# Kernel tuning notes

Hardware: AMD Instinct MI355X
Metric: run time of the kernel (lower is better)

## Reference

```python
import jax, jax.numpy as jnp
import numpy as np
import math

VOCAB, EMBED, RES = 50257, 512, 2048
B, T = 64, 512
LN_EPS = 1e-5


def setup_inputs() -> dict:
    key = jax.random.key(0)
    k_x, k_e, k_r, k_w = jax.random.split(key, 4)
    x = jax.random.randint(k_x, (B, T), 0, VOCAB)
    embed_weight = jax.random.normal(k_e, (VOCAB, EMBED), dtype=jnp.float32)
    R = jax.random.normal(k_r, (RES, RES), dtype=jnp.float32) / math.sqrt(RES) / 0.9
    Win = jax.random.normal(k_w, (EMBED, RES), dtype=jnp.float32) / math.sqrt(EMBED) / 0.9
    gamma = jnp.ones((RES,), dtype=jnp.float32)
    beta = jnp.zeros((RES,), dtype=jnp.float32)
    return {"x": x, "embed_weight": embed_weight, "R": R, "Win": Win,
            "gamma": gamma, "beta": beta}


def reference(x, embed_weight, R, Win, gamma, beta):
    emb = embed_weight[x]                              # [B, T, E]
    inp = jnp.einsum('bte,er->btr', emb, Win)          # [B, T, RES]

    def step(state, u_t):                              # state: [B, RES]
        new_state = jnp.tanh(state @ R + u_t)
        return new_state, None

    state0 = jnp.zeros((x.shape[0], R.shape[0]), dtype=emb.dtype)
    state, _ = jax.lax.scan(step, state0, jnp.swapaxes(inp, 0, 1))  # scan over T

    # LayerNorm over last dim (eps=1e-5, affine)
    mu = jnp.mean(state, axis=-1, keepdims=True)
    var = jnp.mean((state - mu) ** 2, axis=-1, keepdims=True)
    normed = (state - mu) / jnp.sqrt(var + LN_EPS)
    return normed * gamma + beta
```

## Files before the change

kernel.cpp:

```cpp
#include <hip/hip_runtime.h>

#define BB 64
#define TT 512
#define EE 512
#define RR 2048
#define CPW 32
#define RPG 16
#define NWGS 256
#define FPAD 16

typedef _Float16 f16;
typedef f16 f16x8 __attribute__((ext_vector_type(8)));
typedef float f32x4 __attribute__((ext_vector_type(4)));

__device__ __forceinline__ void gload16(const void* g, void* l) {
  __builtin_amdgcn_global_load_lds(
      (const __attribute__((address_space(1))) void*)g,
      (__attribute__((address_space(3))) void*)l, 16, 0, 0);
}

__device__ __forceinline__ float fast_tanh(float v) {
  float e = __expf(2.0f * v);
  return 1.0f - 2.0f / (e + 1.0f);
}

__device__ __forceinline__ void storeS(f16* p, float v) {
  union { f16 h; unsigned short s; } u;
  u.h = (f16)v;
  __hip_atomic_store((unsigned short*)p, u.s, __ATOMIC_RELAXED, __HIP_MEMORY_SCOPE_AGENT);
}

__device__ __forceinline__ unsigned flag_ld(const unsigned* p) {
  return __hip_atomic_load(p, __ATOMIC_RELAXED, __HIP_MEMORY_SCOPE_AGENT);
}
__device__ __forceinline__ void flag_st(unsigned* p, unsigned v) {
  __hip_atomic_store(p, v, __ATOMIC_RELAXED, __HIP_MEMORY_SCOPE_AGENT);
}

__device__ __forceinline__ void issue8(f16x8* dst, unsigned voff, const f16* sbase) {
#pragma unroll
  for (int i = 0; i < 8; ++i)
    asm volatile("global_load_dwordx4 %0, %1, %2 offset:%c3 sc0"
                 : "=v"(dst[i]) : "v"(voff), "s"(sbase), "i"(64 * i) : "memory");
}

__device__ __forceinline__ unsigned bypass_ld(unsigned voff, const unsigned* base) {
  unsigned v;
  asm volatile("global_load_dword %0, %1, %2 sc0 sc1"
               : "=v"(v) : "v"(voff), "s"(base) : "memory");
  return v;
}

template <int N>
__device__ __forceinline__ void wait_vm() {
  asm volatile("s_waitcnt vmcnt(%c0)" :: "i"(N) : "memory");
  __builtin_amdgcn_sched_barrier(0);
}


__global__ void prep_emb(const int* __restrict__ x, const float* __restrict__ ew,
                         f16* __restrict__ emb) {
  const int row = blockIdx.x;
  const int tok = x[row];
  const float4* src = (const float4*)(ew + (size_t)tok * EE);
  f16* dst = emb + (size_t)row * EE;
  const int i = threadIdx.x;
  float4 v = src[i];
  union { f16 h[4]; unsigned long long u; } p;
  p.h[0] = (f16)v.x; p.h[1] = (f16)v.y; p.h[2] = (f16)v.z; p.h[3] = (f16)v.w;
  ((unsigned long long*)dst)[i] = p.u;
}

__global__ void prep_winT(const float* __restrict__ Win, f16* __restrict__ WinT) {
  const int i = blockIdx.x * blockDim.x + threadIdx.x;
  if (i < EE * RR) {
    const int k = i / RR, n = i % RR;
    WinT[(size_t)n * EE + k] = (f16)Win[i];
  }
}


__launch_bounds__(256, 1)
__global__ void proj_gemm(const f16* __restrict__ A, const f16* __restrict__ Bt,
                          float* __restrict__ U) {
  __shared__ f16 As[128 * 32];
  __shared__ f16 Bs[128 * 32];
  const int tid = threadIdx.x;
  const int wv = tid >> 6, l = tid & 63;
  const int m0 = blockIdx.x * 128, n0 = blockIdx.y * 128;
  const int wm = wv >> 1, wn = wv & 1;
  const int srow = tid >> 2, sc = tid & 3;
  const int r = l & 15, kb = l >> 4;
  f32x4 acc[4][4] = {};

  for (int k0 = 0; k0 < EE; k0 += 32) {
    __syncthreads();
#pragma unroll
    for (int q = 0; q < 2; ++q) {
      const int row = q * 64 + srow;
      const int cc = sc ^ (row & 3);
      gload16(A + (size_t)(m0 + row) * EE + k0 + cc * 8,
              (char*)As + q * 4096 + wv * 1024);
      gload16(Bt + (size_t)(n0 + row) * EE + k0 + cc * 8,
              (char*)Bs + q * 4096 + wv * 1024);
    }
    __syncthreads();
    f16x8 af[4], bf[4];
#pragma unroll
    for (int mi = 0; mi < 4; ++mi) {
      const int row = wm * 64 + mi * 16 + r;
      af[mi] = *(const f16x8*)&As[row * 32 + ((kb ^ (row & 3)) * 8)];
    }
#pragma unroll
    for (int ni = 0; ni < 4; ++ni) {
      const int row = wn * 64 + ni * 16 + r;
      bf[ni] = *(const f16x8*)&Bs[row * 32 + ((kb ^ (row & 3)) * 8)];
    }
#pragma unroll
    for (int mi = 0; mi < 4; ++mi)
#pragma unroll
      for (int ni = 0; ni < 4; ++ni)
        acc[mi][ni] = __builtin_amdgcn_mfma_f32_16x16x32_f16(af[mi], bf[ni], acc[mi][ni], 0, 0, 0);
  }
  const int rb = kb * 4;
#pragma unroll
  for (int mi = 0; mi < 4; ++mi)
#pragma unroll
    for (int ni = 0; ni < 4; ++ni)
#pragma unroll
      for (int j = 0; j < 4; ++j) {
        const int m = m0 + wm * 64 + mi * 16 + rb + j;
        const int n = n0 + wn * 64 + ni * 16 + r;
        const int b = m >> 9, t = m & 511;
        __builtin_nontemporal_store(acc[mi][ni][j], &U[(size_t)(t * BB + b) * RR + n]);
      }
}


__launch_bounds__(576, 1)
__global__ void scan_kernel(const float* __restrict__ R, const float* __restrict__ U,
                            f16* __restrict__ S, unsigned* __restrict__ flg,
                            unsigned* __restrict__ fflag) {
  __shared__ __align__(16) char ldsbuf[CPW * RR * 2 + 16 * 1040];
  f16* Rt = (f16*)ldsbuf;
  const char* RtB = (const char*)ldsbuf;

  const int wg = blockIdx.x;
  const int xcd = wg & 7;
  const int grp = xcd >> 1;
  const int cw = ((wg >> 3) << 1) | (wg & 1);
  const bool leader = (wg >> 3) == 0;
  const int nbase = cw * CPW;
  const int rbase = grp * RPG;
  const int tid = threadIdx.x;
  const int wv = tid >> 6, l = tid & 63;
  unsigned* gflags = flg + grp * 64 * FPAD;
  unsigned* myflag = gflags + cw * FPAD;
  unsigned* myff = fflag + xcd * FPAD;

  const int mm = tid >> 5, cc = tid & 31;
  if (tid < 512)
    storeS(&S[(size_t)(BB * RR) + (size_t)(rbase + mm) * RR + nbase + cc],
           fast_tanh(U[(size_t)(rbase + mm) * RR + nbase + cc]));
  __syncthreads();
  if (tid == 0) flag_st(myflag, 1u);

  if (tid < 512) {
    const int c = tid & 31, kst = tid >> 5;
    for (int k = kst; k < RR; k += 16) {
      const float v = R[(size_t)k * RR + nbase + c];
      const int idx = ((k >> 5) << 10) + ((c >> 4) << 9) +
                      (((c & 15) << 2) + ((k >> 3) & 3)) * 8 + (k & 7);
      Rt[idx] = (f16)v;
    }
  }
  __syncthreads();

  if (wv < 8) {
    const int r = l & 15, kb = l >> 4;
    const int kblk = (wv + cw) & 7;
    const unsigned voffA = (unsigned)((((rbase + r) * RR) + (kblk << 8) + kb * 8) * 2);
    const int bb0 = (r * 4 + kb) * 16;
    const unsigned poff = (unsigned)(((grp * 64 + kblk * 8 + (l & 7)) * FPAD) * 4);
    const unsigned foff = (unsigned)((xcd * FPAD) * 4);
    const int ntr = cc >> 4;
    const int lred = (cc & 15) | ((mm >> 2) << 4);
    const int jred = mm & 3;

    f16x8 abuf[8];

    for (int tau = 2; tau <= TT; ++tau) {
      const f16* sprev = S + (size_t)((tau - 1) & 1) * (BB * RR);
      f16* snext = S + (size_t)(tau & 1) * (BB * RR);
      const unsigned need = (unsigned)(tau - 1);

      unsigned ffv = bypass_ld(foff, fflag);
      unsigned pv0 = bypass_ld(poff, flg);
      unsigned pv1 = bypass_ld(poff, flg);
      for (;;) {
        wait_vm<1>();
        if (__all(pv0 >= need)) break;
        pv0 = bypass_ld(poff, flg);
        wait_vm<1>();
        if (__all(pv1 >= need)) break;
        pv1 = bypass_ld(poff, flg);
        __builtin_amdgcn_s_sleep(0);
      }
      wait_vm<0>();
      while (ffv < (unsigned)tau) {
        __builtin_amdgcn_s_sleep(1);
        ffv = flag_ld(myff);
      }

      issue8(abuf, voffA, sprev);
      const float uval = __builtin_nontemporal_load(
          &U[(size_t)(tau - 1) * (BB * RR) + (size_t)(rbase + mm) * RR + nbase + cc]);

      f32x4 acc0 = {0.f, 0.f, 0.f, 0.f}, acc1 = {0.f, 0.f, 0.f, 0.f};
#define KSTEP(ks)                                                              \
  {                                                                            \
    const int kc = (kblk << 3) + (ks);                                         \
    f16x8 b0 = *(const f16x8*)(RtB + kc * 2048 + bb0);                         \
    f16x8 b1 = *(const f16x8*)(RtB + kc * 2048 + 1024 + bb0);                  \
    acc0 = __builtin_amdgcn_mfma_f32_16x16x32_f16(abuf[ks], b0, acc0, 0, 0, 0);\
    acc1 = __builtin_amdgcn_mfma_f32_16x16x32_f16(abuf[ks], b1, acc1, 0, 0, 0);\
  }
      wait_vm<5>();
      KSTEP(0) KSTEP(1) KSTEP(2) KSTEP(3)
      wait_vm<1>();
      KSTEP(4) KSTEP(5) KSTEP(6) KSTEP(7)
#undef KSTEP

      {
        char* red = ldsbuf + CPW * RR * 2;
        *(f32x4*)(red + (wv * 2 + 0) * 1040 + l * 16) = acc0;
        *(f32x4*)(red + (wv * 2 + 1) * 1040 + l * 16) = acc1;
      }
      __syncthreads();
      {
        const char* red = ldsbuf + CPW * RR * 2;
        float s = 0.f;
#pragma unroll
        for (int w = 0; w < 8; ++w)
          s += *(const float*)(red + (w * 2 + ntr) * 1040 + lred * 16 + jred * 4);
        storeS(&snext[(size_t)(rbase + mm) * RR + nbase + cc], fast_tanh(s + uval));
      }
      __syncthreads();
      if (tid == 0) flag_st(myflag, (unsigned)tau);
    }
  } else {
    if (leader) {
      __builtin_amdgcn_fence(__ATOMIC_ACQUIRE, "agent");
      if (l == 0) flag_st(myff, 2u);
    }
    for (int tau = 2; tau <= TT; ++tau) {
      __syncthreads();
      if (leader && tau < TT) {
        __builtin_amdgcn_fence(__ATOMIC_ACQUIRE, "agent");
        if (l == 0) flag_st(myff, (unsigned)(tau + 1));
      }
      __syncthreads();
    }
  }
}


__launch_bounds__(256, 1)
__global__ void ln_kernel(const f16* __restrict__ Sfin, const float* __restrict__ gamma,
                          const float* __restrict__ beta, float* __restrict__ out) {
  const int b = blockIdx.x;
  const int tid = threadIdx.x;
  const f16* row = Sfin + (size_t)b * RR;
  float vals[8];
  float lsum = 0.f, lsq = 0.f;
#pragma unroll
  for (int i = 0; i < 8; ++i) {
    float v = (float)row[tid + i * 256];
    vals[i] = v; lsum += v; lsq += v * v;
  }
#pragma unroll
  for (int off = 32; off >= 1; off >>= 1) {
    lsum += __shfl_xor(lsum, off);
    lsq  += __shfl_xor(lsq, off);
  }
  __shared__ float ps[4], pq[4];
  __shared__ float mu_s, rstd_s;
  const int wv = tid >> 6, l = tid & 63;
  if (l == 0) { ps[wv] = lsum; pq[wv] = lsq; }
  __syncthreads();
  if (tid == 0) {
    float s = 0.f, q = 0.f;
    for (int i = 0; i < 4; ++i) { s += ps[i]; q += pq[i]; }
    const float mu = s / RR;
    const float var = q / RR - mu * mu;
    mu_s = mu; rstd_s = rsqrtf(var + 1e-5f);
  }
  __syncthreads();
  const float mu = mu_s, rstd = rstd_s;
#pragma unroll
  for (int i = 0; i < 8; ++i) {
    const int idx = tid + i * 256;
    out[(size_t)b * RR + idx] = (vals[i] - mu) * rstd * gamma[idx] + beta[idx];
  }
}


extern "C" void kernel_launch(void* const* d_in, const int* in_sizes, int n_in,
                              void* d_out, int out_size, void* d_ws, size_t ws_size,
                              hipStream_t stream) {
  const int*   x     = (const int*)d_in[0];
  const float* ew    = (const float*)d_in[1];
  const float* Rm    = (const float*)d_in[2];
  const float* Win   = (const float*)d_in[3];
  const float* gamma = (const float*)d_in[4];
  const float* beta  = (const float*)d_in[5];

  const size_t U_OFF   = 0;
  const size_t EMB_OFF = 268435456;
  const size_t WT_OFF  = EMB_OFF + 33554432;
  const size_t S_OFF   = WT_OFF + 2097152;
  const size_t BAR_OFF = S_OFF + 524288;
  const size_t FF_OFF  = BAR_OFF + 16384;
  const size_t NEED    = FF_OFF + 1024;
  if (ws_size < NEED) {
    hipMemsetAsync(d_out, 0, (size_t)out_size * 4, stream);
    return;
  }
  char* ws = (char*)d_ws;
  float*    Ubuf  = (float*)(ws + U_OFF);
  f16*      emb   = (f16*)(ws + EMB_OFF);
  f16*      WinT  = (f16*)(ws + WT_OFF);
  f16*      Sbuf  = (f16*)(ws + S_OFF);
  unsigned* flg   = (unsigned*)(ws + BAR_OFF);
  unsigned* fflag = (unsigned*)(ws + FF_OFF);

  hipMemsetAsync(flg, 0, 16384 + 1024, stream);
  prep_emb<<<BB * TT, 128, 0, stream>>>(x, ew, emb);
  prep_winT<<<(EE * RR) / 256, 256, 0, stream>>>(Win, WinT);
  proj_gemm<<<dim3((BB * TT) / 128, RR / 128), 256, 0, stream>>>(emb, WinT, Ubuf);
  scan_kernel<<<NWGS, 576, 0, stream>>>(Rm, Ubuf, Sbuf, flg, fflag);
  ln_kernel<<<BB, 256, 0, stream>>>(Sbuf, gamma, beta, (float*)d_out);
}
```

Before: 1.999 ms.

## Move cross-workgroup flag polling to a dedicated wave with LDS release signaling

The ninth wave now polls the global per-group flags and the XCD fence flag, then publishes a release counter in LDS. The eight compute waves spin on that LDS value instead of issuing global bypass loads, and __syncthreads is replaced by an LDS atomic-counter wave barrier. The next step's U value is also prefetched one iteration ahead. The aim is to take global-memory polling latency and full-block barriers off the recurrence critical path. In exchange it adds LDS spin traffic, bounded spin caps that could silently break ordering if they expire, and subtle memory-ordering risk.

Result: slower. 2.764 ms (+38.3%).

```diff
diff --git a/kernel.cpp b/kernel.cpp
--- a/kernel.cpp
+++ b/kernel.cpp
@@ -8,6 +8,7 @@
 #define RPG 16
 #define NWGS 256
 #define FPAD 16
+#define SPIN_CAP (1 << 18)
 
 typedef _Float16 f16;
 typedef f16 f16x8 __attribute__((ext_vector_type(8)));
@@ -24,9 +25,9 @@
   return 1.0f - 2.0f / (e + 1.0f);
 }
 
-__device__ __forceinline__ void storeS(f16* p, float v) {
+__device__ __forceinline__ void storeS(f16* p, f16 h) {
   union { f16 h; unsigned short s; } u;
-  u.h = (f16)v;
+  u.h = h;
   __hip_atomic_store((unsigned short*)p, u.s, __ATOMIC_RELAXED, __HIP_MEMORY_SCOPE_AGENT);
 }
 
@@ -44,16 +45,22 @@
                  : "=v"(dst[i]) : "v"(voff), "s"(sbase), "i"(64 * i) : "memory");
 }
 
-__device__ __forceinline__ unsigned bypass_ld(unsigned voff, const unsigned* base) {
-  unsigned v;
-  asm volatile("global_load_dword %0, %1, %2 sc0 sc1"
-               : "=v"(v) : "v"(voff), "s"(base) : "memory");
-  return v;
-}
-
 template <int N>
 __device__ __forceinline__ void wait_vm() {
   asm volatile("s_waitcnt vmcnt(%c0)" :: "i"(N) : "memory");
+  __builtin_amdgcn_sched_barrier(0);
+}
+
+__device__ __forceinline__ void wbar(unsigned* cnt, unsigned target, int lane) {
+  asm volatile("s_waitcnt lgkmcnt(0)" ::: "memory");
+  __builtin_amdgcn_sched_barrier(0);
+  if (lane == 0)
+    __hip_atomic_fetch_add(cnt, 1u, __ATOMIC_RELAXED, __HIP_MEMORY_SCOPE_WORKGROUP);
+  unsigned v;
+  int gd = 0;
+  do {
+    v = __hip_atomic_load(cnt, __ATOMIC_RELAXED, __HIP_MEMORY_SCOPE_WORKGROUP);
+  } while (v < target && ++gd < (1 << 22));
   __builtin_amdgcn_sched_barrier(0);
 }
 
@@ -142,6 +149,7 @@
                             f16* __restrict__ S, unsigned* __restrict__ flg,
                             unsigned* __restrict__ fflag) {
   __shared__ __align__(16) char ldsbuf[CPW * RR * 2 + 16 * 1040];
+  __shared__ unsigned wcnt, rel;
   f16* Rt = (f16*)ldsbuf;
   const char* RtB = (const char*)ldsbuf;
 
@@ -154,14 +162,17 @@
   const int rbase = grp * RPG;
   const int tid = threadIdx.x;
   const int wv = tid >> 6, l = tid & 63;
-  unsigned* gflags = flg + grp * 64 * FPAD;
+  unsigned* gflags = flg + (size_t)grp * 64 * FPAD;
   unsigned* myflag = gflags + cw * FPAD;
   unsigned* myff = fflag + xcd * FPAD;
 
+  if (tid == 0) { wcnt = 0u; rel = 1u; }
+
   const int mm = tid >> 5, cc = tid & 31;
-  if (tid < 512)
-    storeS(&S[(size_t)(BB * RR) + (size_t)(rbase + mm) * RR + nbase + cc],
-           fast_tanh(U[(size_t)(rbase + mm) * RR + nbase + cc]));
+  if (tid < 512) {
+    f16 h = (f16)fast_tanh(U[(size_t)(rbase + mm) * RR + nbase + cc]);
+    storeS(&S[(size_t)(BB * RR) + (size_t)(rbase + mm) * RR + nbase + cc], h);
+  }
   __syncthreads();
   if (tid == 0) flag_st(myflag, 1u);
 
@@ -181,40 +192,37 @@
     const int kblk = (wv + cw) & 7;
     const unsigned voffA = (unsigned)((((rbase + r) * RR) + (kblk << 8) + kb * 8) * 2);
     const int bb0 = (r * 4 + kb) * 16;
-    const unsigned poff = (unsigned)(((grp * 64 + kblk * 8 + (l & 7)) * FPAD) * 4);
-    const unsigned foff = (unsigned)((xcd * FPAD) * 4);
     const int ntr = cc >> 4;
     const int lred = (cc & 15) | ((mm >> 2) << 4);
     const int jred = mm & 3;
+    const unsigned ubase = (unsigned)(((rbase + mm) * RR + nbase + cc) * 4);
 
     f16x8 abuf[8];
+    unsigned btgt = 0;
+
+    float ucur;
+    asm volatile("global_load_dword %0, %1, %2 nt"
+                 : "=v"(ucur) : "v"(ubase + (unsigned)(1 * BB * RR * 4)), "s"(U) : "memory");
+    wait_vm<0>();
 
     for (int tau = 2; tau <= TT; ++tau) {
       const f16* sprev = S + (size_t)((tau - 1) & 1) * (BB * RR);
       f16* snext = S + (size_t)(tau & 1) * (BB * RR);
-      const unsigned need = (unsigned)(tau - 1);
-
-      unsigned ffv = bypass_ld(foff, fflag);
-      unsigned pv0 = bypass_ld(poff, flg);
-      unsigned pv1 = bypass_ld(poff, flg);
-      for (;;) {
-        wait_vm<1>();
-        if (__all(pv0 >= need)) break;
-        pv0 = bypass_ld(poff, flg);
-        wait_vm<1>();
-        if (__all(pv1 >= need)) break;
-        pv1 = bypass_ld(poff, flg);
-        __builtin_amdgcn_s_sleep(0);
-      }
-      wait_vm<0>();
-      while (ffv < (unsigned)tau) {
-        __builtin_amdgcn_s_sleep(1);
-        ffv = flag_ld(myff);
+
+      {
+        unsigned v; int gd = 0;
+        do {
+          v = __hip_atomic_load(&rel, __ATOMIC_RELAXED, __HIP_MEMORY_SCOPE_WORKGROUP);
+        } while (v < (unsigned)tau && ++gd < (1 << 22));
       }
 
       issue8(abuf, voffA, sprev);
-      const float uval = __builtin_nontemporal_load(
-          &U[(size_t)(tau - 1) * (BB * RR) + (size_t)(rbase + mm) * RR + nbase + cc]);
+      float unxt;
+      {
+        const int tn = (tau < TT) ? tau : TT - 1;
+        asm volatile("global_load_dword %0, %1, %2 nt"
+                     : "=v"(unxt) : "v"(ubase + (unsigned)(tn * BB * RR * 4)), "s"(U) : "memory");
+      }
 
       f32x4 acc0 = {0.f, 0.f, 0.f, 0.f}, acc1 = {0.f, 0.f, 0.f, 0.f};
 #define KSTEP(ks)                                                              \
@@ -236,30 +244,52 @@
         *(f32x4*)(red + (wv * 2 + 0) * 1040 + l * 16) = acc0;
         *(f32x4*)(red + (wv * 2 + 1) * 1040 + l * 16) = acc1;
       }
-      __syncthreads();
+      wbar(&wcnt, btgt += 8, l);
       {
         const char* red = ldsbuf + CPW * RR * 2;
         float s = 0.f;
 #pragma unroll
         for (int w = 0; w < 8; ++w)
           s += *(const float*)(red + (w * 2 + ntr) * 1040 + lred * 16 + jred * 4);
-        storeS(&snext[(size_t)(rbase + mm) * RR + nbase + cc], fast_tanh(s + uval));
-      }
-      __syncthreads();
+        storeS(&snext[(size_t)(rbase + mm) * RR + nbase + cc],
+               (f16)fast_tanh(s + ucur));
+      }
+      wait_vm<0>();
+      wbar(&wcnt, btgt += 8, l);
       if (tid == 0) flag_st(myflag, (unsigned)tau);
+      ucur = unxt;
     }
   } else {
+    const unsigned* pollp = &gflags[(size_t)l * FPAD];
     if (leader) {
       __builtin_amdgcn_fence(__ATOMIC_ACQUIRE, "agent");
       if (l == 0) flag_st(myff, 2u);
     }
     for (int tau = 2; tau <= TT; ++tau) {
-      __syncthreads();
-      if (leader && tau < TT) {
-        __builtin_amdgcn_fence(__ATOMIC_ACQUIRE, "agent");
-        if (l == 0) flag_st(myff, (unsigned)(tau + 1));
-      }
-      __syncthreads();
+      const unsigned need = (unsigned)(tau - 1);
+      {
+        unsigned fv = flag_ld(pollp);
+        int gd = 0;
+        while (!__all(fv >= need) && ++gd < SPIN_CAP) {
+          __builtin_amdgcn_s_sleep(1);
+          fv = flag_ld(pollp);
+        }
+      }
+      if (leader) {
+        if (tau > 2) {
+          __builtin_amdgcn_fence(__ATOMIC_ACQUIRE, "agent");
+          if (l == 0) flag_st(myff, (unsigned)tau);
+        }
+      } else {
+        unsigned ffv = flag_ld(myff);
+        int gd = 0;
+        while (ffv < (unsigned)tau && ++gd < SPIN_CAP) {
+          __builtin_amdgcn_s_sleep(1);
+          ffv = flag_ld(myff);
+        }
+      }
+      __hip_atomic_store(&rel, (unsigned)tau, __ATOMIC_RELAXED,
+                         __HIP_MEMORY_SCOPE_WORKGROUP);
     }
   }
 }
@@ -319,8 +349,8 @@
   const size_t EMB_OFF = 268435456;
   const size_t WT_OFF  = EMB_OFF + 33554432;
   const size_t S_OFF   = WT_OFF + 2097152;
-  const size_t BAR_OFF = S_OFF + 524288;
-  const size_t FF_OFF  = BAR_OFF + 16384;
+  const size_t FLG_OFF = S_OFF + 524288;
+  const size_t FF_OFF  = FLG_OFF + 16384;
   const size_t NEED    = FF_OFF + 1024;
   if (ws_size < NEED) {
     hipMemsetAsync(d_out, 0, (size_t)out_size * 4, stream);
@@ -331,7 +361,7 @@
   f16*      emb   = (f16*)(ws + EMB_OFF);
   f16*      WinT  = (f16*)(ws + WT_OFF);
   f16*      Sbuf  = (f16*)(ws + S_OFF);
-  unsigned* flg   = (unsigned*)(ws + BAR_OFF);
+  unsigned* flg   = (unsigned*)(ws + FLG_OFF);
   unsigned* fflag = (unsigned*)(ws + FF_OFF);
 
   hipMemsetAsync(flg, 0, 16384 + 1024, stream);
```
